# Optimization experiments

Measured on AMD Instinct MI355X. Metric: run time of the kernel, lower is better.

Reference implementation:

```python
import jax, jax.numpy as jnp
import numpy as np

D_MODEL = 768
N_HEADS = 12
D_HEAD = D_MODEL // N_HEADS
TEMP = float(np.sqrt(D_HEAD))


def setup_inputs() -> dict:
    key = jax.random.key(0)
    ks = jax.random.split(key, 12)
    B, S, D = 8, 2048, D_MODEL
    patches = jax.random.normal(ks[0], (B, S, D), dtype=jnp.float32)
    in_weight = jax.random.uniform(ks[1], (D * 3, D), dtype=jnp.float32)
    in_bias = jax.random.uniform(ks[2], (D * 3,), dtype=jnp.float32)
    out_w = jax.random.normal(ks[3], (D, D), dtype=jnp.float32) * (1.0 / np.sqrt(D))
    out_b = jnp.zeros((D,), dtype=jnp.float32)
    mlp_w1 = jax.random.normal(ks[4], (4 * D, D), dtype=jnp.float32) * (1.0 / np.sqrt(D))
    mlp_b1 = jnp.zeros((4 * D,), dtype=jnp.float32)
    mlp_w2 = jax.random.normal(ks[5], (D, 4 * D), dtype=jnp.float32) * (1.0 / np.sqrt(4 * D))
    mlp_b2 = jnp.zeros((D,), dtype=jnp.float32)
    ln1_g = jnp.ones((D,), dtype=jnp.float32)
    ln1_b = jnp.zeros((D,), dtype=jnp.float32)
    ln2_g = jnp.ones((D,), dtype=jnp.float32)
    ln2_b = jnp.zeros((D,), dtype=jnp.float32)
    return {
        "patches": patches,
        "in_weight": in_weight, "in_bias": in_bias,
        "out_w": out_w, "out_b": out_b,
        "mlp_w1": mlp_w1, "mlp_b1": mlp_b1,
        "mlp_w2": mlp_w2, "mlp_b2": mlp_b2,
        "ln1_g": ln1_g, "ln1_b": ln1_b,
        "ln2_g": ln2_g, "ln2_b": ln2_b,
    }


def layer_norm(x, g, b, eps=1e-5):
    mu = jnp.mean(x, axis=-1, keepdims=True)
    var = jnp.var(x, axis=-1, keepdims=True)
    return (x - mu) * jax.lax.rsqrt(var + eps) * g + b


def mha(x, in_weight, in_bias, out_w, out_b):
    # Replicate quirky per-head reshape: [3D, D] -> [H, d_head, 3, D]
    W = in_weight.reshape(N_HEADS, D_HEAD, 3, D_MODEL)  # h, e, 3, d
    Bv = in_bias.reshape(N_HEADS, D_HEAD, 3)            # h, e, 3
    qw, kw, vw = W[:, :, 0, :], W[:, :, 1, :], W[:, :, 2, :]  # [H, e, D]
    qb, kb, vb = Bv[:, :, 0], Bv[:, :, 1], Bv[:, :, 2]        # [H, e]
    # Q,K,V per head: [B, H, S, e]
    Q = jnp.einsum('bsd,hed->bhse', x, qw) + qb[None, :, None, :]
    K = jnp.einsum('bsd,hed->bhse', x, kw) + kb[None, :, None, :]
    V = jnp.einsum('bsd,hed->bhse', x, vw) + vb[None, :, None, :]
    atn = jnp.einsum('bhse,bhte->bhst', Q, K)
    atn = jax.nn.softmax(atn / TEMP, axis=-1)
    # NOTE: original uses V (not atn @ V) as head output; heads concatenated over feature dim
    B_, H, S, e = V.shape
    heads = jnp.transpose(V, (0, 2, 1, 3)).reshape(B_, S, H * e)
    masks = jnp.sum(atn, axis=1)  # sum over heads: [B, S, S]
    out = heads @ out_w.T + out_b
    return out, masks


def reference(patches, in_weight, in_bias, out_w, out_b,
              mlp_w1, mlp_b1, mlp_w2, mlp_b2,
              ln1_g, ln1_b, ln2_g, ln2_b):
    x = layer_norm(patches, ln1_g, ln1_b)
    sa, _ = mha(x, in_weight, in_bias, out_w, out_b)
    x = sa + x  # dropout = identity (eval)
    x = layer_norm(x, ln2_g, ln2_b)
    h = jax.nn.selu(x @ mlp_w1.T + mlp_b1)
    x = (h @ mlp_w2.T + mlp_b2) + x
    return x
```

## Files before the change

kernel.cpp:

```cpp
#include <hip/hip_runtime.h>


typedef __bf16 bf16;
typedef __bf16 bf16x8 __attribute__((ext_vector_type(8)));
typedef __bf16 bf16x4 __attribute__((ext_vector_type(4)));
typedef float  f32x4  __attribute__((ext_vector_type(4)));

#define N_ROWS  16384

#define AS1(p) ((const __attribute__((address_space(1))) void*)(p))
#define AS3(p) ((__attribute__((address_space(3))) void*)(p))

#define VM6 0x0F76
#define VM3 0x0F73
#define VM0 0x0F70

#define N1 589824
#define N2 589824
#define N3 147456
__global__ __launch_bounds__(256) void prep_cast(const float* __restrict__ w1,
                                                 const float* __restrict__ w2,
                                                 const float* __restrict__ ow,
                                                 bf16* __restrict__ w1b,
                                                 bf16* __restrict__ w2b,
                                                 bf16* __restrict__ owb) {
  int i = blockIdx.x * 256 + threadIdx.x;
  const float* src; bf16* dst; int off;
  if (i < N1)           { src = w1; dst = w1b; off = i; }
  else if (i < N1 + N2) { src = w2; dst = w2b; off = i - N1; }
  else                  { src = ow; dst = owb; off = i - N1 - N2; }
  float4 v = ((const float4*)src)[off];
  bf16x4 o = {(bf16)v.x, (bf16)v.y, (bf16)v.z, (bf16)v.w};
  *(bf16x4*)(dst + 4 * (size_t)off) = o;
}

__global__ __launch_bounds__(256) void wvt_kernel(const float* __restrict__ in_weight,
                                                  bf16* __restrict__ wvt) {
  __shared__ float t[64][65];
  const int k0 = blockIdx.x * 64, j0 = blockIdx.y * 64;
  const int tx = threadIdx.x & 63, ty = threadIdx.x >> 6;
  for (int jj = ty; jj < 64; jj += 4)
    t[jj][tx] = in_weight[((size_t)(j0 + jj) * 3 + 2) * 768 + k0 + tx];
  __syncthreads();
  for (int kk = ty; kk < 64; kk += 4)
    wvt[(size_t)(k0 + kk) * 768 + j0 + tx] = (bf16)t[tx][kk];
}

__global__ __launch_bounds__(64) void bias_combine_kernel(const float* __restrict__ out_w,
                                                          const float* __restrict__ in_bias,
                                                          const float* __restrict__ out_b,
                                                          float* __restrict__ bc) {
  int n = blockIdx.x, l = threadIdx.x;
  float s = 0.f;
  for (int j = l; j < 768; j += 64) s += out_w[(size_t)n * 768 + j] * in_bias[j * 3 + 2];
#pragma unroll
  for (int off = 32; off > 0; off >>= 1) s += __shfl_xor(s, off, 64);
  if (l == 0) bc[n] = s + out_b[n];
}

template <typename TIN>
__global__ __launch_bounds__(256) void ln_kernel(const TIN* __restrict__ x,
                                                 const float* __restrict__ g,
                                                 const float* __restrict__ b,
                                                 bf16* __restrict__ y) {
  const int row = blockIdx.x;
  const TIN* xr = x + (size_t)row * 768;
  float v[3], s1 = 0.f, s2 = 0.f;
#pragma unroll
  for (int i = 0; i < 3; ++i) {
    v[i] = (float)xr[threadIdx.x + i * 256];
    s1 += v[i];
    s2 += v[i] * v[i];
  }
#pragma unroll
  for (int off = 32; off > 0; off >>= 1) {
    s1 += __shfl_xor(s1, off, 64);
    s2 += __shfl_xor(s2, off, 64);
  }
  __shared__ float red[8];
  int w = threadIdx.x >> 6, l = threadIdx.x & 63;
  if (l == 0) { red[w * 2] = s1; red[w * 2 + 1] = s2; }
  __syncthreads();
  s1 = red[0] + red[2] + red[4] + red[6];
  s2 = red[1] + red[3] + red[5] + red[7];
  const float mu = s1 * (1.f / 768.f);
  const float var = s2 * (1.f / 768.f) - mu * mu;
  const float rstd = rsqrtf(var + 1e-5f);
#pragma unroll
  for (int i = 0; i < 3; ++i) {
    int d = threadIdx.x + i * 256;
    y[(size_t)row * 768 + d] = (bf16)((v[i] - mu) * rstd * g[d] + b[d]);
  }
}

#define SLOT_E (384 * 32)
template <int EPI>
__global__ __launch_bounds__(512, 2) void gemm_bt(const bf16* __restrict__ A,
                                                  const bf16* __restrict__ B,
                                                  const float* __restrict__ bias,
                                                  const bf16* __restrict__ resid,
                                                  void* __restrict__ out,
                                                  int M, int N, int K) {
  __shared__ bf16 ring[4 * SLOT_E];
  const int tid = threadIdx.x;
  const int w = tid >> 6, l = tid & 63;
  const int wr = w >> 2, wcn = w & 3;
  const int q = l >> 4, m16 = l & 15;

  int mtile, ntile;
  {
    const int L = blockIdx.y * gridDim.x + blockIdx.x;
    const int gy = gridDim.y;
    if ((gy & 7) == 0) {
      const int mpx = gy >> 3;
      const int xcd = L & 7;
      const int slot = L >> 3;
      mtile = xcd * mpx + (slot % mpx);
      ntile = slot / mpx;
    } else {
      mtile = blockIdx.y; ntile = blockIdx.x;
    }
  }
  const long tileM = (long)mtile * 128;
  const long tileN = (long)ntile * 256;

  const int rowA = tid >> 2;
  const int clA = ((tid & 3) - (rowA >> 1)) & 3;
  const bf16* gA = A + (tileM + rowA) * (long)K + clA * 8;
  const int ldA = tid * 8;
  const bf16* gB[2]; int ldB[2];
#pragma unroll
  for (int j = 0; j < 2; ++j) {
    const int ch = tid + j * 512;
    const int row = ch >> 2;
    const int cl = ((ch & 3) - (row >> 1)) & 3;
    gB[j] = B + (tileN + row) * (long)K + cl * 8;
    ldB[j] = ch * 8;
  }

  int offA[4], offB[4];
#pragma unroll
  for (int mi = 0; mi < 4; ++mi) {
    const int r = wr * 64 + mi * 16 + m16;
    offA[mi] = r * 32 + (((q + (r >> 1)) & 3) << 3);
  }
#pragma unroll
  for (int ni = 0; ni < 4; ++ni) {
    const int r = wcn * 64 + ni * 16 + m16;
    offB[ni] = r * 32 + (((q + (r >> 1)) & 3) << 3);
  }

  f32x4 acc[4][4] = {};

#pragma unroll
  for (int s = 0; s < 3; ++s) {
    bf16* da = ring + s * SLOT_E;
    bf16* db = da + 128 * 32;
    __builtin_amdgcn_global_load_lds(AS1(gA + s * 32), AS3(&da[ldA]), 16, 0, 0);
#pragma unroll
    for (int j = 0; j < 2; ++j)
      __builtin_amdgcn_global_load_lds(AS1(gB[j] + s * 32), AS3(&db[ldB[j]]), 16, 0, 0);
  }
  long k_next = 96;

#define KSTEP(SLOT, WIMM, ISSUE)                                               \
  {                                                                            \
    __builtin_amdgcn_s_waitcnt(WIMM);                                          \
    __builtin_amdgcn_s_barrier();                                              \
    if (ISSUE) {                                                               \
      bf16* da = ring + (((SLOT) + 3) & 3) * SLOT_E;                           \
      bf16* db = da + 128 * 32;                                                \
      __builtin_amdgcn_global_load_lds(AS1(gA + k_next), AS3(&da[ldA]), 16, 0, 0); \
      _Pragma("unroll")                                                        \
      for (int j = 0; j < 2; ++j)                                              \
        __builtin_amdgcn_global_load_lds(AS1(gB[j] + k_next), AS3(&db[ldB[j]]), 16, 0, 0); \
      k_next += 32;                                                            \
    }                                                                          \
    const bf16* ca = ring + (SLOT) * SLOT_E;                                   \
    const bf16* cb = ca + 128 * 32;                                            \
    bf16x8 bfr[4];                                                             \
    _Pragma("unroll")                                                          \
    for (int ni = 0; ni < 4; ++ni) bfr[ni] = *(const bf16x8*)&cb[offB[ni]];    \
    _Pragma("unroll")                                                          \
    for (int mi = 0; mi < 4; ++mi) {                                           \
      const bf16x8 af = *(const bf16x8*)&ca[offA[mi]];                         \
      _Pragma("unroll")                                                        \
      for (int ni = 0; ni < 4; ++ni)                                           \
        acc[mi][ni] = __builtin_amdgcn_mfma_f32_16x16x32_bf16(af, bfr[ni],     \
                                                              acc[mi][ni], 0, 0, 0); \
    }                                                                          \
  }

  const int T = K >> 5;
#pragma unroll 1
  for (int g = 0; g < T - 4; g += 4) {
    KSTEP(0, VM6, 1) KSTEP(1, VM6, 1) KSTEP(2, VM6, 1) KSTEP(3, VM6, 1)
  }
  KSTEP(0, VM6, 1) KSTEP(1, VM6, 0) KSTEP(2, VM3, 0) KSTEP(3, VM0, 0)
#undef KSTEP

  const long colBase = tileN + (long)wcn * 64 + m16;
  const long rowBase = tileM + (long)wr * 64 + q * 4;
#pragma unroll
  for (int mi = 0; mi < 4; ++mi) {
#pragma unroll
    for (int r = 0; r < 4; ++r) {
      const long row = rowBase + mi * 16 + r;
#pragma unroll
      for (int ni = 0; ni < 4; ++ni) {
        const long col = colBase + ni * 16;
        float v = acc[mi][ni][r];
        if (EPI == 0) {
          ((bf16*)out)[row * N + col] = (bf16)v;
        } else if (EPI == 1) {
          v += bias[col] + (float)resid[row * N + col];
          ((float*)out)[row * N + col] = v;
        } else if (EPI == 2) {
          v += bias[col];
          v = v > 0.f ? 1.0507009873554805f * v
                      : 1.0507009873554805f * 1.6732632423543772f * (__expf(v) - 1.f);
          ((bf16*)out)[row * N + col] = (bf16)v;
        } else {
          v += bias[col] + (float)resid[row * N + col];
          ((bf16*)out)[row * N + col] = (bf16)v;
        }
      }
    }
  }
}

extern "C" void kernel_launch(void* const* d_in, const int* in_sizes, int n_in,
                              void* d_out, int out_size, void* d_ws, size_t ws_size,
                              hipStream_t stream) {
  const float* patches   = (const float*)d_in[0];
  const float* in_weight = (const float*)d_in[1];
  const float* in_bias   = (const float*)d_in[2];
  const float* out_w     = (const float*)d_in[3];
  const float* out_b     = (const float*)d_in[4];
  const float* mlp_w1    = (const float*)d_in[5];
  const float* mlp_b1    = (const float*)d_in[6];
  const float* mlp_w2    = (const float*)d_in[7];
  const float* mlp_b2    = (const float*)d_in[8];
  const float* ln1_g     = (const float*)d_in[9];
  const float* ln1_b     = (const float*)d_in[10];
  const float* ln2_g     = (const float*)d_in[11];
  const float* ln2_b     = (const float*)d_in[12];

  char* ws = (char*)d_ws;
  const size_t MB = 1024 * 1024;
  bf16* Wc   = (bf16*)(ws + 0);
  bf16* w1b  = (bf16*)(ws + 2 * MB);
  bf16* w2b  = (bf16*)(ws + 8 * MB);
  bf16* owb  = (bf16*)(ws + 14 * MB);
  bf16* wvt  = (bf16*)(ws + 16 * MB);
  float* bc  = (float*)(ws + 18 * MB);
  bf16* X1   = (bf16*)(ws + 20 * MB);
  bf16* X3   = (bf16*)(ws + 20 * MB);
  bf16* X2b  = (bf16*)(ws + 48 * MB);
  bf16* H    = (bf16*)(ws + 48 * MB);

  prep_cast<<<(N1 + N2 + N3) / 256, 256, 0, stream>>>(mlp_w1, mlp_w2, out_w,
                                                      w1b, w2b, owb);
  wvt_kernel<<<dim3(12, 12), 256, 0, stream>>>(in_weight, wvt);
  bias_combine_kernel<<<768, 64, 0, stream>>>(out_w, in_bias, out_b, bc);
  gemm_bt<0><<<dim3(3, 6), 512, 0, stream>>>(owb, wvt, nullptr, nullptr, Wc, 768, 768, 768);

  ln_kernel<float><<<N_ROWS, 256, 0, stream>>>(patches, ln1_g, ln1_b, X1);
  gemm_bt<3><<<dim3(3, 128), 512, 0, stream>>>(X1, Wc, bc, X1, X2b, N_ROWS, 768, 768);
  ln_kernel<bf16><<<N_ROWS, 256, 0, stream>>>(X2b, ln2_g, ln2_b, X3);
  gemm_bt<2><<<dim3(12, 128), 512, 0, stream>>>(X3, w1b, mlp_b1, nullptr, H, N_ROWS, 3072, 768);
  gemm_bt<1><<<dim3(3, 128), 512, 0, stream>>>(H, w2b, mlp_b2, X3, d_out, N_ROWS, 768, 3072);
}
```

Measured before the change: 399.6 us.

## Enlarge GEMM tile to 256x256 with double-buffered 64-wide K phases

Rewrites the bf16 GEMM to compute 256x256 output tiles per 512-thread block, with each wave holding 8x4 MFMA accumulators. The 4-slot ring of 32-wide K slices becomes a two-buffer scheme of 64-wide K stages, loaded in quarter-phases interleaved with compute. Fragment loads are hoisted ahead of barriers, and s_setprio is raised around the MFMA bursts. The aim is higher arithmetic intensity per LDS and global byte, at the cost of 128 KB of LDS, more accumulator registers, more barriers, and half as many blocks, which reduces occupancy and tail balance.

```diff
diff --git a/kernel.cpp b/kernel.cpp
--- a/kernel.cpp
+++ b/kernel.cpp
@@ -11,8 +11,7 @@
 #define AS1(p) ((const __attribute__((address_space(1))) void*)(p))
 #define AS3(p) ((__attribute__((address_space(3))) void*)(p))
 
-#define VM6 0x0F76
-#define VM3 0x0F73
+#define VM4 0x0F74
 #define VM0 0x0F70
 
 #define N1 589824
@@ -93,7 +92,6 @@
   }
 }
 
-#define SLOT_E (384 * 32)
 template <int EPI>
 __global__ __launch_bounds__(512, 2) void gemm_bt(const bf16* __restrict__ A,
                                                   const bf16* __restrict__ B,
@@ -101,7 +99,7 @@
                                                   const bf16* __restrict__ resid,
                                                   void* __restrict__ out,
                                                   int M, int N, int K) {
-  __shared__ bf16 ring[4 * SLOT_E];
+  __shared__ bf16 ring[65536];
   const int tid = threadIdx.x;
   const int w = tid >> 6, l = tid & 63;
   const int wr = w >> 2, wcn = w & 3;
@@ -121,88 +119,115 @@
       mtile = blockIdx.y; ntile = blockIdx.x;
     }
   }
-  const long tileM = (long)mtile * 128;
+  const long tileM = (long)mtile * 256;
   const long tileN = (long)ntile * 256;
 
-  const int rowA = tid >> 2;
-  const int clA = ((tid & 3) - (rowA >> 1)) & 3;
-  const bf16* gA = A + (tileM + rowA) * (long)K + clA * 8;
-  const int ldA = tid * 8;
-  const bf16* gB[2]; int ldB[2];
-#pragma unroll
-  for (int j = 0; j < 2; ++j) {
-    const int ch = tid + j * 512;
-    const int row = ch >> 2;
-    const int cl = ((ch & 3) - (row >> 1)) & 3;
-    gB[j] = B + (tileN + row) * (long)K + cl * 8;
-    ldB[j] = ch * 8;
-  }
-
-  int offA[4], offB[4];
-#pragma unroll
-  for (int mi = 0; mi < 4; ++mi) {
-    const int r = wr * 64 + mi * 16 + m16;
-    offA[mi] = r * 32 + (((q + (r >> 1)) & 3) << 3);
-  }
+  const bf16* gA[2][2]; const bf16* gB[2][2];
+  int lA[2][2], lB[2][2];
+  {
+    const int sc = l & 3;
+#pragma unroll
+    for (int j = 0; j < 2; ++j) {
+      const int b = w * 2 + j;
+      const int p = b >> 3, s = (b >> 2) & 1, blk = b & 3;
+#pragma unroll
+      for (int mh = 0; mh < 2; ++mh) {
+        const int row = s * 128 + mh * 64 + blk * 16 + (l >> 2);
+        const int cl = (sc - (row >> 1)) & 3;
+        gA[mh][j] = A + (tileM + row) * (long)K + p * 32 + cl * 8;
+        lA[mh][j] = p * 8192 + row * 32 + sc * 8;
+      }
+      const int rowB = b * 16 + (l >> 2);
+      const int clB = (sc - (rowB >> 1)) & 3;
+#pragma unroll
+      for (int ks = 0; ks < 2; ++ks) {
+        gB[ks][j] = B + (tileN + rowB) * (long)K + ks * 32 + clB * 8;
+        lB[ks][j] = 16384 + ks * 8192 + rowB * 32 + sc * 8;
+      }
+    }
+  }
+
+  int offA[8], offB[4];
+#pragma unroll
+  for (int mh = 0; mh < 2; ++mh)
+#pragma unroll
+    for (int mi = 0; mi < 4; ++mi) {
+      const int r = wr * 128 + mh * 64 + mi * 16 + m16;
+      offA[mh * 4 + mi] = r * 32 + (((q + (r >> 1)) & 3) << 3);
+    }
 #pragma unroll
   for (int ni = 0; ni < 4; ++ni) {
     const int r = wcn * 64 + ni * 16 + m16;
     offB[ni] = r * 32 + (((q + (r >> 1)) & 3) << 3);
   }
 
-  f32x4 acc[4][4] = {};
-
-#pragma unroll
-  for (int s = 0; s < 3; ++s) {
-    bf16* da = ring + s * SLOT_E;
-    bf16* db = da + 128 * 32;
-    __builtin_amdgcn_global_load_lds(AS1(gA + s * 32), AS3(&da[ldA]), 16, 0, 0);
-#pragma unroll
-    for (int j = 0; j < 2; ++j)
-      __builtin_amdgcn_global_load_lds(AS1(gB[j] + s * 32), AS3(&db[ldB[j]]), 16, 0, 0);
-  }
-  long k_next = 96;
-
-#define KSTEP(SLOT, WIMM, ISSUE)                                               \
+  f32x4 acc[8][4] = {};
+
+#define ST(GP, LO, BUF)                                                        \
+  { bf16* bb = ring + (BUF) * 32768;                                           \
+    __builtin_amdgcn_global_load_lds(AS1(GP[0]), AS3(bb + LO[0]), 16, 0, 0);   \
+    __builtin_amdgcn_global_load_lds(AS1(GP[1]), AS3(bb + LO[1]), 16, 0, 0);   \
+    GP[0] += 64; GP[1] += 64; }
+
+  ST(gA[0], lA[0], 0) ST(gB[0], lB[0], 0) ST(gA[1], lA[1], 0) ST(gB[1], lB[1], 0)
+  ST(gA[0], lA[0], 1) ST(gB[0], lB[0], 1)
+  __builtin_amdgcn_s_waitcnt(VM4);
+  __builtin_amdgcn_s_barrier();
+
+#define PHASE(BUF, MH, KS, STG, DOVM, VMW)                                     \
   {                                                                            \
-    __builtin_amdgcn_s_waitcnt(WIMM);                                          \
+    const bf16* pa = ring + (BUF) * 32768 + (KS) * 8192;                       \
+    const bf16* pb = ring + (BUF) * 32768 + 16384 + (KS) * 8192;               \
+    bf16x8 af[4], bv[4];                                                       \
+    _Pragma("unroll")                                                          \
+    for (int mi = 0; mi < 4; ++mi)                                             \
+      af[mi] = *(const bf16x8*)&pa[offA[(MH) * 4 + mi]];                       \
+    _Pragma("unroll")                                                          \
+    for (int ni = 0; ni < 4; ++ni)                                             \
+      bv[ni] = *(const bf16x8*)&pb[offB[ni]];                                  \
+    STG;                                                                       \
+    if (DOVM) __builtin_amdgcn_s_waitcnt(VMW);                                 \
     __builtin_amdgcn_s_barrier();                                              \
-    if (ISSUE) {                                                               \
-      bf16* da = ring + (((SLOT) + 3) & 3) * SLOT_E;                           \
-      bf16* db = da + 128 * 32;                                                \
-      __builtin_amdgcn_global_load_lds(AS1(gA + k_next), AS3(&da[ldA]), 16, 0, 0); \
-      _Pragma("unroll")                                                        \
-      for (int j = 0; j < 2; ++j)                                              \
-        __builtin_amdgcn_global_load_lds(AS1(gB[j] + k_next), AS3(&db[ldB[j]]), 16, 0, 0); \
-      k_next += 32;                                                            \
-    }                                                                          \
-    const bf16* ca = ring + (SLOT) * SLOT_E;                                   \
-    const bf16* cb = ca + 128 * 32;                                            \
-    bf16x8 bfr[4];                                                             \
-    _Pragma("unroll")                                                          \
-    for (int ni = 0; ni < 4; ++ni) bfr[ni] = *(const bf16x8*)&cb[offB[ni]];    \
+    asm volatile("s_waitcnt lgkmcnt(0)");                                      \
+    __builtin_amdgcn_s_setprio(1);                                             \
     _Pragma("unroll")                                                          \
     for (int mi = 0; mi < 4; ++mi) {                                           \
-      const bf16x8 af = *(const bf16x8*)&ca[offA[mi]];                         \
       _Pragma("unroll")                                                        \
       for (int ni = 0; ni < 4; ++ni)                                           \
-        acc[mi][ni] = __builtin_amdgcn_mfma_f32_16x16x32_bf16(af, bfr[ni],     \
-                                                              acc[mi][ni], 0, 0, 0); \
+        acc[(MH) * 4 + mi][ni] = __builtin_amdgcn_mfma_f32_16x16x32_bf16(      \
+            af[mi], bv[ni], acc[(MH) * 4 + mi][ni], 0, 0, 0);                  \
     }                                                                          \
-  }
-
-  const int T = K >> 5;
+    __builtin_amdgcn_s_setprio(0);                                             \
+    __builtin_amdgcn_s_barrier();                                              \
+  }
+
+  const int T = K >> 6;
 #pragma unroll 1
-  for (int g = 0; g < T - 4; g += 4) {
-    KSTEP(0, VM6, 1) KSTEP(1, VM6, 1) KSTEP(2, VM6, 1) KSTEP(3, VM6, 1)
-  }
-  KSTEP(0, VM6, 1) KSTEP(1, VM6, 0) KSTEP(2, VM3, 0) KSTEP(3, VM0, 0)
-#undef KSTEP
+  for (int i = 0; i < T / 2 - 1; ++i) {
+    PHASE(0, 0, 0, ST(gA[1], lA[1], 1), 0, VM0)
+    PHASE(0, 0, 1, ST(gB[1], lB[1], 1), 0, VM0)
+    PHASE(0, 1, 0, ST(gA[0], lA[0], 0), 0, VM0)
+    PHASE(0, 1, 1, ST(gB[0], lB[0], 0), 1, VM4)
+    PHASE(1, 0, 0, ST(gA[1], lA[1], 0), 0, VM0)
+    PHASE(1, 0, 1, ST(gB[1], lB[1], 0), 0, VM0)
+    PHASE(1, 1, 0, ST(gA[0], lA[0], 1), 0, VM0)
+    PHASE(1, 1, 1, ST(gB[0], lB[0], 1), 1, VM4)
+  }
+  PHASE(0, 0, 0, ST(gA[1], lA[1], 1), 0, VM0)
+  PHASE(0, 0, 1, ST(gB[1], lB[1], 1), 0, VM0)
+  PHASE(0, 1, 0, (void)0, 0, VM0)
+  PHASE(0, 1, 1, (void)0, 1, VM0)
+  PHASE(1, 0, 0, (void)0, 0, VM0)
+  PHASE(1, 0, 1, (void)0, 0, VM0)
+  PHASE(1, 1, 0, (void)0, 0, VM0)
+  PHASE(1, 1, 1, (void)0, 0, VM0)
+#undef PHASE
+#undef ST
 
   const long colBase = tileN + (long)wcn * 64 + m16;
-  const long rowBase = tileM + (long)wr * 64 + q * 4;
-#pragma unroll
-  for (int mi = 0; mi < 4; ++mi) {
+  const long rowBase = tileM + (long)wr * 128 + q * 4;
+#pragma unroll
+  for (int mi = 0; mi < 8; ++mi) {
 #pragma unroll
     for (int r = 0; r < 4; ++r) {
       const long row = rowBase + mi * 16 + r;
@@ -263,11 +288,11 @@
                                                       w1b, w2b, owb);
   wvt_kernel<<<dim3(12, 12), 256, 0, stream>>>(in_weight, wvt);
   bias_combine_kernel<<<768, 64, 0, stream>>>(out_w, in_bias, out_b, bc);
-  gemm_bt<0><<<dim3(3, 6), 512, 0, stream>>>(owb, wvt, nullptr, nullptr, Wc, 768, 768, 768);
+  gemm_bt<0><<<dim3(3, 3), 512, 0, stream>>>(owb, wvt, nullptr, nullptr, Wc, 768, 768, 768);
 
   ln_kernel<float><<<N_ROWS, 256, 0, stream>>>(patches, ln1_g, ln1_b, X1);
-  gemm_bt<3><<<dim3(3, 128), 512, 0, stream>>>(X1, Wc, bc, X1, X2b, N_ROWS, 768, 768);
+  gemm_bt<3><<<dim3(3, 64), 512, 0, stream>>>(X1, Wc, bc, X1, X2b, N_ROWS, 768, 768);
   ln_kernel<bf16><<<N_ROWS, 256, 0, stream>>>(X2b, ln2_g, ln2_b, X3);
-  gemm_bt<2><<<dim3(12, 128), 512, 0, stream>>>(X3, w1b, mlp_b1, nullptr, H, N_ROWS, 3072, 768);
-  gemm_bt<1><<<dim3(3, 128), 512, 0, stream>>>(H, w2b, mlp_b2, X3, d_out, N_ROWS, 768, 3072);
-}
+  gemm_bt<2><<<dim3(12, 64), 512, 0, stream>>>(X3, w1b, mlp_b1, nullptr, H, N_ROWS, 3072, 768);
+  gemm_bt<1><<<dim3(3, 64), 512, 0, stream>>>(H, w2b, mlp_b2, X3, d_out, N_ROWS, 768, 3072);
+}
```

Result: no change. 396.6 us (-0.7%).
